# Kernel optimization log

Hardware: AMD Instinct MI355X
Metric: run time of the kernel (lower is better)

Reference implementation:

```python
import jax, jax.numpy as jnp
import numpy as np

N_NODES = 100000
N_EDGES = 1600000
IN_DIM = 128
HID_DIM = 64
OUT_DIM = 128
EPS = 1e-5


def setup_inputs() -> dict:
    key = jax.random.key(0)
    ks = jax.random.split(key, 10)
    feat = jax.random.normal(ks[0], (N_NODES, IN_DIM), dtype=jnp.float32)
    src = jax.random.randint(ks[1], (N_EDGES,), 0, N_NODES)
    dst = jax.random.randint(ks[2], (N_EDGES,), 0, N_NODES)
    # learned params
    gamma = jnp.ones((IN_DIM,), jnp.float32)
    beta = jnp.zeros((IN_DIM,), jnp.float32)
    Wq = jax.random.normal(ks[3], (IN_DIM, HID_DIM), jnp.float32) * 0.05
    bq = jax.random.normal(ks[4], (HID_DIM,), jnp.float32) * 0.05
    Wk = jax.random.normal(ks[5], (IN_DIM, HID_DIM), jnp.float32) * 0.05
    Wv = jax.random.normal(ks[6], (IN_DIM, OUT_DIM), jnp.float32) * 0.05
    We = jax.random.normal(ks[7], (HID_DIM, 1), jnp.float32) * 0.05
    return {"feat": feat, "src": src, "dst": dst, "gamma": gamma, "beta": beta,
            "Wq": Wq, "bq": bq, "Wk": Wk, "Wv": Wv, "We": We}


def reference(feat, src, dst, gamma, beta, Wq, bq, Wk, Wv, We):
    # BatchNorm1d (training-mode batch stats, biased variance)
    mean = jnp.mean(feat, axis=0)
    var = jnp.mean((feat - mean) ** 2, axis=0)
    x = (feat - mean) * jax.lax.rsqrt(var + EPS) * gamma + beta
    # feat_drop = 0.0 -> identity
    q = x @ Wq + bq          # [N, H]
    k = x @ Wk               # [N, H]
    v = x @ Wv               # [N, O]
    # u_add_v: src-node q + dst-node k per edge, then sigmoid and fc_e -> scalar score
    e = jax.nn.sigmoid(q[src] + k[dst]) @ We  # [E, 1]
    e = e[:, 0]                               # [E]
    # edge_softmax: softmax over incoming edges of each destination node
    m = jax.ops.segment_max(e, dst, num_segments=N_NODES)  # [N]
    ex = jnp.exp(e - m[dst])
    s = jax.ops.segment_sum(ex, dst, num_segments=N_NODES)  # [N]
    a = ex / s[dst]                                          # [E]
    # u_mul_e_sum: weighted scatter-sum of source v into destinations
    rst = jax.ops.segment_sum(v[src] * a[:, None], dst, num_segments=N_NODES)  # [N, O]
    return rst
```

## Files before the change

### kernel.cpp

```cpp
#include <hip/hip_runtime.h>
#include <math.h>

#define IN_DIM 128
#define HID 64
#define OUT_DIM 128
#define ELL_W 64
#define BKT 32
#define HWG 64
constexpr float EPS = 1e-5f;

typedef short short8 __attribute__((ext_vector_type(8)));
typedef float f32x4  __attribute__((ext_vector_type(4)));


__device__ inline ushort f2bf(float x) {
    __bf16 h = (__bf16)x;
    return *reinterpret_cast<ushort*>(&h);
}
__device__ inline short f2bfs(float x) {
    __bf16 h = (__bf16)x;
    return *reinterpret_cast<short*>(&h);
}
__device__ inline float bf2f(ushort u) {
    union { unsigned u; float f; } c; c.u = ((unsigned)u) << 16;
    return c.f;
}
__device__ inline float4 bf4_to_f4(ushort4 u) {
    return make_float4(bf2f(u.x), bf2f(u.y), bf2f(u.z), bf2f(u.w));
}

__global__ __launch_bounds__(256) void pre_kernel(
    const float* __restrict__ feat, float* __restrict__ ws, int n_nodes,
    const int* __restrict__ dst, int* __restrict__ bcnt, int n_edges,
    const float* __restrict__ Wq, const float* __restrict__ Wk,
    const float* __restrict__ Wv, ushort* __restrict__ Bfrag,
    int nbk, int chunk)
{
    extern __shared__ int sm[];
    int t = threadIdx.x;

    if (blockIdx.x < 256) {
        float* redS = (float*)sm;
        float* redQ = redS + 256;
        int col  = t & 127;
        int half = t >> 7;
        float sum = 0.f, sq = 0.f;
        for (int r = blockIdx.x * 2 + half; r < n_nodes; r += 512) {
            float x = feat[r * IN_DIM + col];
            sum += x; sq += x * x;
        }
        redS[t] = sum; redQ[t] = sq;
        __syncthreads();
        if (t < 128) {
            sum = redS[t] + redS[t + 128];
            sq  = redQ[t] + redQ[t + 128];
            unsafeAtomicAdd(&ws[col], sum);
            unsafeAtomicAdd(&ws[128 + col], sq);
        }
    } else if (blockIdx.x < 256 + HWG) {
        int w = blockIdx.x - 256;
        for (int b = t; b < nbk; b += 256) sm[b] = 0;
        __syncthreads();
        int lo = w * chunk;
        int hi = lo + chunk; if (hi > n_edges) hi = n_edges;
        for (int e = lo + t; e < hi; e += 256)
            atomicAdd(&sm[__builtin_nontemporal_load(dst + e) >> 5], 1);
        __syncthreads();
        for (int b = t; b < nbk; b += 256)
            if (sm[b]) atomicAdd(&bcnt[b], sm[b]);
    } else {
        int gid  = (blockIdx.x - 256 - HWG) * 256 + t;
        int f    = gid >> 6;
        int lane = gid & 63;
        int kc = f & 3, ct = (f >> 2) & 3, w = f >> 4;
        int col   = w * 64 + ct * 16 + (lane & 15);
        int kbase = kc * 32 + (lane >> 4) * 8;
        ushort tmp[8];
        #pragma unroll
        for (int j = 0; j < 8; j++) {
            int k = kbase + j;
            float val;
            if (col < 64)       val = Wq[k * HID + col];
            else if (col < 128) val = Wk[k * HID + (col - 64)];
            else                val = Wv[k * OUT_DIM + (col - 128)];
            tmp[j] = f2bf(val);
        }
        ushort* d = &Bfrag[(f * 64 + lane) * 8];
        *(ushort4*)d       = make_ushort4(tmp[0], tmp[1], tmp[2], tmp[3]);
        *(ushort4*)(d + 4) = make_ushort4(tmp[4], tmp[5], tmp[6], tmp[7]);
    }
}

__global__ __launch_bounds__(256) void scan_init(
    const int* __restrict__ bcnt, int* __restrict__ offs,
    int* __restrict__ cursor, int n)
{
    __shared__ int tmp[256];
    int t = threadIdx.x;
    int base = 0;
    for (int i0 = 0; i0 < n; i0 += 256) {
        int i = i0 + t;
        int d = (i < n) ? bcnt[i] : 0;
        tmp[t] = d; __syncthreads();
        for (int s = 1; s < 256; s <<= 1) {
            int cur = tmp[t];
            int add = (t >= s) ? tmp[t - s] : 0;
            __syncthreads();
            tmp[t] = cur + add;
            __syncthreads();
        }
        int excl = tmp[t] - d;
        if (i < n) { offs[i] = base + excl; cursor[i] = base + excl; }
        base += tmp[255];
        __syncthreads();
    }
    if (t == 0) offs[n] = base;
}

__global__ __launch_bounds__(512) void scatter_bins(
    const int* __restrict__ src, const int* __restrict__ dst,
    int* __restrict__ cursor, int* __restrict__ packed,
    int n_edges, int nbk, int chunk)
{
    extern __shared__ int sm[];
    int* cnt  = sm;
    int* base = sm + nbk;
    int w = blockIdx.x, t = threadIdx.x;
    for (int b = t; b < nbk; b += 512) cnt[b] = 0;
    __syncthreads();
    int lo = w * chunk;
    int hi = lo + chunk; if (hi > n_edges) hi = n_edges;
    for (int e = lo + t; e < hi; e += 512)
        atomicAdd(&cnt[__builtin_nontemporal_load(dst + e) >> 5], 1);
    __syncthreads();
    for (int b = t; b < nbk; b += 512) {
        int c = cnt[b];
        if (c) base[b] = atomicAdd(&cursor[b], c);
        cnt[b] = 0;
    }
    __syncthreads();
    for (int e = lo + t; e < hi; e += 512) {
        int d = __builtin_nontemporal_load(dst + e);
        int s = __builtin_nontemporal_load(src + e);
        int b = d >> 5;
        int pos = base[b] + atomicAdd(&cnt[b], 1);
        packed[pos] = (int)(((unsigned)(d & 31) << 26) | (unsigned)s);
    }
}

__global__ __launch_bounds__(256) void mfma_qkv(
    const float* __restrict__ feat, const ushort* __restrict__ Bfrag,
    const float* __restrict__ bq,
    const float* __restrict__ gamma, const float* __restrict__ beta,
    const float* __restrict__ stats,
    ushort* __restrict__ qvb, ushort* __restrict__ kb,
    int n_nodes)
{
    __shared__ float sc[IN_DIM], sh[IN_DIM];
    int tid = threadIdx.x;
    if (tid < 128) {
        float inv_n = 1.0f / (float)n_nodes;
        float mean = stats[tid] * inv_n;
        float var  = stats[128 + tid] * inv_n - mean * mean;
        float s    = gamma[tid] * rsqrtf(var + EPS);
        sc[tid] = s; sh[tid] = beta[tid] - mean * s;
    }

    int w    = tid >> 6;
    int lane = tid & 63;
    int row0 = blockIdx.x * 64;
    int m    = lane & 15;
    int quad = lane >> 4;
    int nm1  = n_nodes - 1;

    short8 bfr[16];
    #pragma unroll
    for (int f = 0; f < 16; f++)
        bfr[f] = *(const short8*)&Bfrag[((w * 16 + f) * 64 + lane) * 8];

    __syncthreads();

    f32x4 acc[4][4] = {};

    #pragma unroll
    for (int kc = 0; kc < 4; kc++) {
        int koff = kc * 32 + quad * 8;
        float4 sc0 = *(const float4*)&sc[koff];
        float4 sc1 = *(const float4*)&sc[koff + 4];
        float4 sh0 = *(const float4*)&sh[koff];
        float4 sh1 = *(const float4*)&sh[koff + 4];
        short8 afr[4];
        #pragma unroll
        for (int rt = 0; rt < 4; rt++) {
            int row = row0 + rt * 16 + m;
            row = row < nm1 ? row : nm1;
            const float* fp = &feat[(size_t)row * IN_DIM + koff];
            float4 x0 = *(const float4*)fp;
            float4 x1 = *(const float4*)(fp + 4);
            afr[rt][0] = f2bfs(x0.x * sc0.x + sh0.x);
            afr[rt][1] = f2bfs(x0.y * sc0.y + sh0.y);
            afr[rt][2] = f2bfs(x0.z * sc0.z + sh0.z);
            afr[rt][3] = f2bfs(x0.w * sc0.w + sh0.w);
            afr[rt][4] = f2bfs(x1.x * sc1.x + sh1.x);
            afr[rt][5] = f2bfs(x1.y * sc1.y + sh1.y);
            afr[rt][6] = f2bfs(x1.z * sc1.z + sh1.z);
            afr[rt][7] = f2bfs(x1.w * sc1.w + sh1.w);
        }
        #pragma unroll
        for (int rt = 0; rt < 4; rt++)
            #pragma unroll
            for (int ct = 0; ct < 4; ct++)
                acc[rt][ct] = __builtin_amdgcn_mfma_f32_16x16x32_bf16(
                    afr[rt], bfr[ct * 4 + kc], acc[rt][ct], 0, 0, 0);
    }

    ushort* base; int ld, cl;
    if (w == 1)      { base = kb;  ld = HID; cl = 0; }
    else             { base = qvb; ld = 192; cl = (w == 0) ? 0 : 64 * (w - 1); }

    #pragma unroll
    for (int ct = 0; ct < 4; ct++) {
        int col = cl + ct * 16 + m;
        float bias = (w == 0) ? bq[ct * 16 + m] : 0.f;
        #pragma unroll
        for (int rt = 0; rt < 4; rt++) {
            int r0 = row0 + rt * 16 + quad * 4;
            #pragma unroll
            for (int r = 0; r < 4; r++)
                base[(size_t)(r0 + r) * ld + col] = f2bf(acc[rt][ct][r] + bias);
        }
    }
}

__device__ __forceinline__ void gather_core(
    const int* row, int cnt, int node, int h, int sub,
    const ushort* __restrict__ qvb, const ushort* __restrict__ kb,
    const float* __restrict__ We, float* __restrict__ out)
{
    if (cnt == 0) {
        if (sub == 0) {
            float4 z = make_float4(0.f, 0.f, 0.f, 0.f);
            *(float4*)&out[node * OUT_DIM + 4 * h]      = z;
            *(float4*)&out[node * OUT_DIM + 64 + 4 * h] = z;
        }
        return;
    }

    float4 kd = bf4_to_f4(*(const ushort4*)&kb[node * HID + 4 * h]);
    float4 we = *(const float4*)&We[4 * h];

    float4 o0 = make_float4(0.f, 0.f, 0.f, 0.f);
    float4 o1 = make_float4(0.f, 0.f, 0.f, 0.f);
    float ssum = 0.f;

    for (int p0 = 0; p0 < cnt; p0 += 4) {
        int p = p0 + sub;
        bool act = (p < cnt);
        int sN = row[act ? p : 0];
        const ushort* qv = qvb + (size_t)sN * 192;
        float4 qq = bf4_to_f4(*(const ushort4*)(qv + 4 * h));
        float t;
        t  = we.x * __fdividef(1.f, 1.f + __expf(-(qq.x + kd.x)));
        t += we.y * __fdividef(1.f, 1.f + __expf(-(qq.y + kd.y)));
        t += we.z * __fdividef(1.f, 1.f + __expf(-(qq.z + kd.z)));
        t += we.w * __fdividef(1.f, 1.f + __expf(-(qq.w + kd.w)));
        t += __shfl_xor(t, 1);
        t += __shfl_xor(t, 2);
        t += __shfl_xor(t, 4);
        t += __shfl_xor(t, 8);
        float exv = act ? __expf(t) : 0.f;
        ssum += exv;
        float4 v0 = bf4_to_f4(*(const ushort4*)(qv + 64 + 4 * h));
        float4 v1 = bf4_to_f4(*(const ushort4*)(qv + 128 + 4 * h));
        o0.x += exv * v0.x; o0.y += exv * v0.y;
        o0.z += exv * v0.z; o0.w += exv * v0.w;
        o1.x += exv * v1.x; o1.y += exv * v1.y;
        o1.z += exv * v1.z; o1.w += exv * v1.w;
    }

    ssum += __shfl_xor(ssum, 16); ssum += __shfl_xor(ssum, 32);
    o0.x += __shfl_xor(o0.x, 16); o0.x += __shfl_xor(o0.x, 32);
    o0.y += __shfl_xor(o0.y, 16); o0.y += __shfl_xor(o0.y, 32);
    o0.z += __shfl_xor(o0.z, 16); o0.z += __shfl_xor(o0.z, 32);
    o0.w += __shfl_xor(o0.w, 16); o0.w += __shfl_xor(o0.w, 32);
    o1.x += __shfl_xor(o1.x, 16); o1.x += __shfl_xor(o1.x, 32);
    o1.y += __shfl_xor(o1.y, 16); o1.y += __shfl_xor(o1.y, 32);
    o1.z += __shfl_xor(o1.z, 16); o1.z += __shfl_xor(o1.z, 32);
    o1.w += __shfl_xor(o1.w, 16); o1.w += __shfl_xor(o1.w, 32);

    if (sub == 0) {
        float inv = (ssum > 0.f) ? __fdividef(1.f, ssum) : 0.f;
        o0.x *= inv; o0.y *= inv; o0.z *= inv; o0.w *= inv;
        o1.x *= inv; o1.y *= inv; o1.z *= inv; o1.w *= inv;
        *(float4*)&out[node * OUT_DIM + 4 * h]      = o0;
        *(float4*)&out[node * OUT_DIM + 64 + 4 * h] = o1;
    }
}

__global__ __launch_bounds__(256) void gather_fused(
    const int* __restrict__ offs, const int* __restrict__ packed,
    const ushort* __restrict__ qvb, const ushort* __restrict__ kb,
    const float* __restrict__ We,
    float* __restrict__ out, int n_nodes)
{
    __shared__ int deg_l[BKT];
    __shared__ int ell_l[BKT][ELL_W];
    int b = blockIdx.x;
    int t = threadIdx.x;
    if (t < BKT) deg_l[t] = 0;
    __syncthreads();

    int beg = offs[b];
    int end = offs[b + 1];
    for (int e = beg + t; e < end; e += 256) {
        int p = packed[e];
        int dl = (int)((unsigned)p >> 26);
        int pos = atomicAdd(&deg_l[dl], 1);
        if (pos < ELL_W) ell_l[dl][pos] = p & 0x03FFFFFF;
    }
    __syncthreads();

    int wv   = t >> 6;
    int lane = t & 63;
    int h    = lane & 15;
    int sub  = lane >> 4;
    #pragma unroll 1
    for (int i = 0; i < BKT / 4; i++) {
        int dl = wv * (BKT / 4) + i;
        int node = b * BKT + dl;
        if (node >= n_nodes) break;
        int cnt = deg_l[dl];
        cnt = cnt < ELL_W ? cnt : ELL_W;
        gather_core(&ell_l[dl][0], cnt, node, h, sub, qvb, kb, We, out);
    }
}

extern "C" void kernel_launch(void* const* d_in, const int* in_sizes, int n_in,
                              void* d_out, int out_size, void* d_ws, size_t ws_size,
                              hipStream_t stream)
{
    const float* feat  = (const float*)d_in[0];
    const int*   src   = (const int*)d_in[1];
    const int*   dst   = (const int*)d_in[2];
    const float* gamma = (const float*)d_in[3];
    const float* beta  = (const float*)d_in[4];
    const float* Wq    = (const float*)d_in[5];
    const float* bq    = (const float*)d_in[6];
    const float* Wk    = (const float*)d_in[7];
    const float* Wv    = (const float*)d_in[8];
    const float* We    = (const float*)d_in[9];

    int n_nodes = in_sizes[0] / IN_DIM;
    int n_edges = in_sizes[1];
    int n_pad   = n_nodes + 64;
    int nbk     = (n_nodes + BKT - 1) / BKT;
    int chunk   = (n_edges + HWG - 1) / HWG;

    float* ws = (float*)d_ws;

    int* bcnt   = (int*)(ws + 256);
    int* offs   = bcnt + nbk;
    int* cursor = offs + nbk + 1;
    int* packed = cursor + nbk;
    size_t off = 256 + (size_t)nbk + (nbk + 1) + nbk + (size_t)n_edges;
    off = (off + 3) & ~(size_t)3;
    ushort* qvb   = (ushort*)(ws + off);
    ushort* kb    = qvb + (size_t)n_pad * 192;
    ushort* Bfrag = kb + (size_t)n_pad * HID;

    size_t lds_pre  = (size_t)(nbk > 512 ? nbk : 512) * sizeof(int);
    size_t lds_scat = 2 * (size_t)nbk * sizeof(int);

    hipMemsetAsync(ws, 0, (256 + (size_t)nbk) * sizeof(float), stream);
    pre_kernel<<<256 + HWG + 16, 256, lds_pre, stream>>>(
        feat, ws, n_nodes, dst, bcnt, n_edges, Wq, Wk, Wv, Bfrag, nbk, chunk);
    scan_init<<<1, 256, 0, stream>>>(bcnt, offs, cursor, nbk);
    scatter_bins<<<HWG, 512, lds_scat, stream>>>(
        src, dst, cursor, packed, n_edges, nbk, chunk);
    mfma_qkv<<<(n_nodes + 63) / 64, 256, 0, stream>>>(
        feat, Bfrag, bq, gamma, beta, ws, qvb, kb, n_nodes);
    gather_fused<<<nbk, 256, 0, stream>>>(
        offs, packed, qvb, kb, We, (float*)d_out, n_nodes);
}
```

Measured before the change: 429.7 us.

## Replace bucketed CSR build with global-atomic ELL fill overlapped with QKV GEMM

Removes the histogram, scan and bucket-scatter kernels and instead builds a per-node ELL table directly with global atomics on per-node degree counters. The edge fill is split across two launches: part runs beside the BN-stats kernel and the rest runs as extra blocks inside the MFMA QKV kernel, so it overlaps compute. The gather kernel now reads the global ELL rows with one wavefront per node, and exp is replaced by exp2 with the log2(e) factor folded into We. Costs are heavy global atomic contention and scattered ELL writes. Edge order within a node becomes nondeterministic, so float summation order can vary between runs.

```diff
diff --git a/kernel.cpp b/kernel.cpp
--- a/kernel.cpp
+++ b/kernel.cpp
@@ -5,12 +5,13 @@
 #define HID 64
 #define OUT_DIM 128
 #define ELL_W 64
-#define BKT 32
-#define HWG 64
+#define FA 512
+#define FB 512
 constexpr float EPS = 1e-5f;
 
 typedef short short8 __attribute__((ext_vector_type(8)));
 typedef float f32x4  __attribute__((ext_vector_type(4)));
+typedef int   i32x4  __attribute__((ext_vector_type(4)));
 
 
 __device__ inline ushort f2bf(float x) {
@@ -29,19 +30,44 @@
     return make_float4(bf2f(u.x), bf2f(u.y), bf2f(u.z), bf2f(u.w));
 }
 
-__global__ __launch_bounds__(256) void pre_kernel(
+__device__ __forceinline__ void fill_edges(
+    const int* __restrict__ src, const int* __restrict__ dst,
+    int* __restrict__ deg, int* __restrict__ ell,
+    int e0, int e1, int bid, int nblk)
+{
+    int idx    = bid * 256 + threadIdx.x;
+    int stride = nblk * 256;
+    int nv     = (e1 - e0) >> 2;
+    const i32x4* d4p = reinterpret_cast<const i32x4*>(dst + e0);
+    const i32x4* s4p = reinterpret_cast<const i32x4*>(src + e0);
+
+    for (int i = idx; i < nv; i += stride) {
+        i32x4 d4 = __builtin_nontemporal_load(d4p + i);
+        i32x4 s4 = __builtin_nontemporal_load(s4p + i);
+        #pragma unroll
+        for (int j = 0; j < 4; j++) {
+            int d = d4[j];
+            int pos = atomicAdd(&deg[d], 1);
+            if (pos < ELL_W) ell[(size_t)d * ELL_W + pos] = s4[j];
+        }
+    }
+    for (int e = e0 + (nv << 2) + idx; e < e1; e += stride) {
+        int d = dst[e];
+        int pos = atomicAdd(&deg[d], 1);
+        if (pos < ELL_W) ell[(size_t)d * ELL_W + pos] = src[e];
+    }
+}
+
+__global__ __launch_bounds__(256) void preA(
     const float* __restrict__ feat, float* __restrict__ ws, int n_nodes,
-    const int* __restrict__ dst, int* __restrict__ bcnt, int n_edges,
     const float* __restrict__ Wq, const float* __restrict__ Wk,
     const float* __restrict__ Wv, ushort* __restrict__ Bfrag,
-    int nbk, int chunk)
-{
-    extern __shared__ int sm[];
+    const int* __restrict__ src, const int* __restrict__ dst,
+    int* __restrict__ deg, int* __restrict__ ell, int e1)
+{
     int t = threadIdx.x;
-
     if (blockIdx.x < 256) {
-        float* redS = (float*)sm;
-        float* redQ = redS + 256;
+        __shared__ float redS[256], redQ[256];
         int col  = t & 127;
         int half = t >> 7;
         float sum = 0.f, sq = 0.f;
@@ -57,19 +83,8 @@
             unsafeAtomicAdd(&ws[col], sum);
             unsafeAtomicAdd(&ws[128 + col], sq);
         }
-    } else if (blockIdx.x < 256 + HWG) {
-        int w = blockIdx.x - 256;
-        for (int b = t; b < nbk; b += 256) sm[b] = 0;
-        __syncthreads();
-        int lo = w * chunk;
-        int hi = lo + chunk; if (hi > n_edges) hi = n_edges;
-        for (int e = lo + t; e < hi; e += 256)
-            atomicAdd(&sm[__builtin_nontemporal_load(dst + e) >> 5], 1);
-        __syncthreads();
-        for (int b = t; b < nbk; b += 256)
-            if (sm[b]) atomicAdd(&bcnt[b], sm[b]);
-    } else {
-        int gid  = (blockIdx.x - 256 - HWG) * 256 + t;
+    } else if (blockIdx.x < 256 + 16) {
+        int gid  = (blockIdx.x - 256) * 256 + t;
         int f    = gid >> 6;
         int lane = gid & 63;
         int kc = f & 3, ct = (f >> 2) & 3, w = f >> 4;
@@ -88,74 +103,26 @@
         ushort* d = &Bfrag[(f * 64 + lane) * 8];
         *(ushort4*)d       = make_ushort4(tmp[0], tmp[1], tmp[2], tmp[3]);
         *(ushort4*)(d + 4) = make_ushort4(tmp[4], tmp[5], tmp[6], tmp[7]);
-    }
-}
-
-__global__ __launch_bounds__(256) void scan_init(
-    const int* __restrict__ bcnt, int* __restrict__ offs,
-    int* __restrict__ cursor, int n)
-{
-    __shared__ int tmp[256];
-    int t = threadIdx.x;
-    int base = 0;
-    for (int i0 = 0; i0 < n; i0 += 256) {
-        int i = i0 + t;
-        int d = (i < n) ? bcnt[i] : 0;
-        tmp[t] = d; __syncthreads();
-        for (int s = 1; s < 256; s <<= 1) {
-            int cur = tmp[t];
-            int add = (t >= s) ? tmp[t - s] : 0;
-            __syncthreads();
-            tmp[t] = cur + add;
-            __syncthreads();
-        }
-        int excl = tmp[t] - d;
-        if (i < n) { offs[i] = base + excl; cursor[i] = base + excl; }
-        base += tmp[255];
-        __syncthreads();
-    }
-    if (t == 0) offs[n] = base;
-}
-
-__global__ __launch_bounds__(512) void scatter_bins(
-    const int* __restrict__ src, const int* __restrict__ dst,
-    int* __restrict__ cursor, int* __restrict__ packed,
-    int n_edges, int nbk, int chunk)
-{
-    extern __shared__ int sm[];
-    int* cnt  = sm;
-    int* base = sm + nbk;
-    int w = blockIdx.x, t = threadIdx.x;
-    for (int b = t; b < nbk; b += 512) cnt[b] = 0;
-    __syncthreads();
-    int lo = w * chunk;
-    int hi = lo + chunk; if (hi > n_edges) hi = n_edges;
-    for (int e = lo + t; e < hi; e += 512)
-        atomicAdd(&cnt[__builtin_nontemporal_load(dst + e) >> 5], 1);
-    __syncthreads();
-    for (int b = t; b < nbk; b += 512) {
-        int c = cnt[b];
-        if (c) base[b] = atomicAdd(&cursor[b], c);
-        cnt[b] = 0;
-    }
-    __syncthreads();
-    for (int e = lo + t; e < hi; e += 512) {
-        int d = __builtin_nontemporal_load(dst + e);
-        int s = __builtin_nontemporal_load(src + e);
-        int b = d >> 5;
-        int pos = base[b] + atomicAdd(&cnt[b], 1);
-        packed[pos] = (int)(((unsigned)(d & 31) << 26) | (unsigned)s);
-    }
-}
-
-__global__ __launch_bounds__(256) void mfma_qkv(
+    } else {
+        fill_edges(src, dst, deg, ell, 0, e1, blockIdx.x - 272, FA);
+    }
+}
+
+__global__ __launch_bounds__(256) void fusedB(
     const float* __restrict__ feat, const ushort* __restrict__ Bfrag,
     const float* __restrict__ bq,
     const float* __restrict__ gamma, const float* __restrict__ beta,
     const float* __restrict__ stats,
-    ushort* __restrict__ qvb, ushort* __restrict__ kb,
-    int n_nodes)
-{
+    ushort* __restrict__ qvb, ushort* __restrict__ kb, int n_nodes,
+    const int* __restrict__ src, const int* __restrict__ dst,
+    int* __restrict__ deg, int* __restrict__ ell, int e1, int n_edges,
+    int mb)
+{
+    if (blockIdx.x >= mb) {
+        fill_edges(src, dst, deg, ell, e1, n_edges, blockIdx.x - mb, FB);
+        return;
+    }
+
     __shared__ float sc[IN_DIM], sh[IN_DIM];
     int tid = threadIdx.x;
     if (tid < 128) {
@@ -232,11 +199,20 @@
     }
 }
 
-__device__ __forceinline__ void gather_core(
-    const int* row, int cnt, int node, int h, int sub,
+__global__ __launch_bounds__(256) void gather_ell(
+    const int* __restrict__ deg, const int* __restrict__ ell,
     const ushort* __restrict__ qvb, const ushort* __restrict__ kb,
-    const float* __restrict__ We, float* __restrict__ out)
-{
+    const float* __restrict__ We,
+    float* __restrict__ out, int n_nodes)
+{
+    int node = (blockIdx.x * 256 + threadIdx.x) >> 6;
+    int lane = threadIdx.x & 63;
+    if (node >= n_nodes) return;
+    int h   = lane & 15;
+    int sub = lane >> 4;
+    int cnt = deg[node];
+    cnt = cnt < ELL_W ? cnt : ELL_W;
+
     if (cnt == 0) {
         if (sub == 0) {
             float4 z = make_float4(0.f, 0.f, 0.f, 0.f);
@@ -246,8 +222,11 @@
         return;
     }
 
+    const int* row = &ell[(size_t)node * ELL_W];
     float4 kd = bf4_to_f4(*(const ushort4*)&kb[node * HID + 4 * h]);
     float4 we = *(const float4*)&We[4 * h];
+    const float L2E = 1.4426950408889634f;
+    we.x *= L2E; we.y *= L2E; we.z *= L2E; we.w *= L2E;
 
     float4 o0 = make_float4(0.f, 0.f, 0.f, 0.f);
     float4 o1 = make_float4(0.f, 0.f, 0.f, 0.f);
@@ -268,7 +247,7 @@
         t += __shfl_xor(t, 2);
         t += __shfl_xor(t, 4);
         t += __shfl_xor(t, 8);
-        float exv = act ? __expf(t) : 0.f;
+        float exv = act ? exp2f(t) : 0.f;
         ssum += exv;
         float4 v0 = bf4_to_f4(*(const ushort4*)(qv + 64 + 4 * h));
         float4 v1 = bf4_to_f4(*(const ushort4*)(qv + 128 + 4 * h));
@@ -294,44 +273,6 @@
         o1.x *= inv; o1.y *= inv; o1.z *= inv; o1.w *= inv;
         *(float4*)&out[node * OUT_DIM + 4 * h]      = o0;
         *(float4*)&out[node * OUT_DIM + 64 + 4 * h] = o1;
-    }
-}
-
-__global__ __launch_bounds__(256) void gather_fused(
-    const int* __restrict__ offs, const int* __restrict__ packed,
-    const ushort* __restrict__ qvb, const ushort* __restrict__ kb,
-    const float* __restrict__ We,
-    float* __restrict__ out, int n_nodes)
-{
-    __shared__ int deg_l[BKT];
-    __shared__ int ell_l[BKT][ELL_W];
-    int b = blockIdx.x;
-    int t = threadIdx.x;
-    if (t < BKT) deg_l[t] = 0;
-    __syncthreads();
-
-    int beg = offs[b];
-    int end = offs[b + 1];
-    for (int e = beg + t; e < end; e += 256) {
-        int p = packed[e];
-        int dl = (int)((unsigned)p >> 26);
-        int pos = atomicAdd(&deg_l[dl], 1);
-        if (pos < ELL_W) ell_l[dl][pos] = p & 0x03FFFFFF;
-    }
-    __syncthreads();
-
-    int wv   = t >> 6;
-    int lane = t & 63;
-    int h    = lane & 15;
-    int sub  = lane >> 4;
-    #pragma unroll 1
-    for (int i = 0; i < BKT / 4; i++) {
-        int dl = wv * (BKT / 4) + i;
-        int node = b * BKT + dl;
-        if (node >= n_nodes) break;
-        int cnt = deg_l[dl];
-        cnt = cnt < ELL_W ? cnt : ELL_W;
-        gather_core(&ell_l[dl][0], cnt, node, h, sub, qvb, kb, We, out);
     }
 }
 
@@ -353,32 +294,26 @@
     int n_nodes = in_sizes[0] / IN_DIM;
     int n_edges = in_sizes[1];
     int n_pad   = n_nodes + 64;
-    int nbk     = (n_nodes + BKT - 1) / BKT;
-    int chunk   = (n_edges + HWG - 1) / HWG;
+    int mb      = (n_nodes + 63) / 64;
+    int e1      = ((n_edges * 9) / 20) & ~3;
 
     float* ws = (float*)d_ws;
 
-    int* bcnt   = (int*)(ws + 256);
-    int* offs   = bcnt + nbk;
-    int* cursor = offs + nbk + 1;
-    int* packed = cursor + nbk;
-    size_t off = 256 + (size_t)nbk + (nbk + 1) + nbk + (size_t)n_edges;
+    int* deg = (int*)(ws + 256);
+    int* ell = deg + n_nodes;
+    size_t off = 256 + (size_t)n_nodes * (1 + ELL_W);
     off = (off + 3) & ~(size_t)3;
     ushort* qvb   = (ushort*)(ws + off);
     ushort* kb    = qvb + (size_t)n_pad * 192;
     ushort* Bfrag = kb + (size_t)n_pad * HID;
 
-    size_t lds_pre  = (size_t)(nbk > 512 ? nbk : 512) * sizeof(int);
-    size_t lds_scat = 2 * (size_t)nbk * sizeof(int);
-
-    hipMemsetAsync(ws, 0, (256 + (size_t)nbk) * sizeof(float), stream);
-    pre_kernel<<<256 + HWG + 16, 256, lds_pre, stream>>>(
-        feat, ws, n_nodes, dst, bcnt, n_edges, Wq, Wk, Wv, Bfrag, nbk, chunk);
-    scan_init<<<1, 256, 0, stream>>>(bcnt, offs, cursor, nbk);
-    scatter_bins<<<HWG, 512, lds_scat, stream>>>(
-        src, dst, cursor, packed, n_edges, nbk, chunk);
-    mfma_qkv<<<(n_nodes + 63) / 64, 256, 0, stream>>>(
-        feat, Bfrag, bq, gamma, beta, ws, qvb, kb, n_nodes);
-    gather_fused<<<nbk, 256, 0, stream>>>(
-        offs, packed, qvb, kb, We, (float*)d_out, n_nodes);
-}
+    hipMemsetAsync(ws, 0, (256 + (size_t)n_nodes) * sizeof(float), stream);
+    preA<<<256 + 16 + FA, 256, 0, stream>>>(
+        feat, ws, n_nodes, Wq, Wk, Wv, Bfrag, src, dst, deg, ell, e1);
+    fusedB<<<mb + FB, 256, 0, stream>>>(
+        feat, Bfrag, bq, gamma, beta, ws, qvb, kb, n_nodes,
+        src, dst, deg, ell, e1, n_edges, mb);
+    long long g_threads = (long long)n_nodes * 64;
+    gather_ell<<<(int)((g_threads + 255) / 256), 256, 0, stream>>>(
+        deg, ell, qvb, kb, We, (float*)d_out, n_nodes);
+}
```

After: 409.5 us. 4.7% less time.
